# Performance work log

Measured on AMD Instinct MI355X. Metric: run time of the kernel, lower is better.

Reference implementation:

```python
import jax, jax.numpy as jnp
import numpy as np

N_EMBED = 16384
EMBED_DIM = 256
BETA = 1.0  # default forward arg


def setup_inputs() -> dict:
    key = jax.random.key(0)
    k1, k2 = jax.random.split(key)
    z = jax.random.normal(k1, (8, EMBED_DIM, 32, 32), dtype=jnp.float32)
    # nn.Embedding init: uniform(-1/n_embed, 1/n_embed)
    embed_w = jax.random.uniform(k2, (N_EMBED, EMBED_DIM), dtype=jnp.float32,
                                 minval=-1.0 / N_EMBED, maxval=1.0 / N_EMBED)
    return {"z": z, "embed_w": embed_w}


def reference(z, embed_w):
    B, C, H, W = z.shape
    zb = jnp.transpose(z, (0, 2, 3, 1))            # (B,H,W,C)
    zf = zb.reshape(B * H * W, C)                  # (BHW, C)
    # squared L2 distances to every code: ||z||^2 + ||e||^2 - 2 z.e
    d = (jnp.sum(zf ** 2, axis=1, keepdims=True)
         + jnp.sum(embed_w ** 2, axis=1)
         - 2.0 * jnp.einsum('bd,nd->bn', zf, embed_w))  # (BHW, n_embed)
    idx = jnp.argmin(d, axis=1)                    # (BHW,)
    z_q = embed_w[idx].reshape(B, H, W, C)         # codebook gather
    loss = (BETA * jnp.mean((jax.lax.stop_gradient(z_q) - zb) ** 2)
            + jnp.mean((z_q - jax.lax.stop_gradient(zb)) ** 2))
    # straight-through estimator
    z_q = zb + jax.lax.stop_gradient(z_q - zb)
    z_q = jnp.transpose(z_q, (0, 3, 1, 2))         # (B,C,H,W)
    return z_q, loss
```

## Files before the change

kernel.cpp:

```cpp
#include <hip/hip_runtime.h>
#include <hip/hip_bf16.h>
#include <stdint.h>


typedef __attribute__((ext_vector_type(8))) short bf16x8;
typedef __attribute__((ext_vector_type(8))) unsigned short ushort8v;
typedef __attribute__((ext_vector_type(4))) float f32x4;

__device__ __forceinline__ unsigned short f2bf(float f) {
  unsigned u = __float_as_uint(f);
  return (unsigned short)((u + 0x7FFFu + ((u >> 16) & 1u)) >> 16);
}

typedef const __attribute__((address_space(1))) unsigned char* gas1;
typedef __attribute__((address_space(3))) unsigned char* las3;
__device__ __forceinline__ void cp16(const void* g, void* l) {
  __builtin_amdgcn_global_load_lds((gas1)g, (las3)l, 16, 0, 0);
}

__global__ void k_prep(const float* __restrict__ z, const float* __restrict__ ew,
                       unsigned short* __restrict__ zp, unsigned short* __restrict__ ep,
                       float* __restrict__ h2, float* __restrict__ out) {
  __shared__ float tile[32][132];
  int bid = blockIdx.x;
  int t = threadIdx.x;
  if (bid < 512) {
    int b = bid >> 6, ct = (bid >> 3) & 7, hwt = bid & 7;
    const float* src = z + b * 262144 + ct * 32768 + hwt * 128;
#pragma unroll
    for (int it = 0; it < 4; ++it) {
      int cell = it * 1024 + t * 4;
      int cl = cell >> 7, hl = cell & 127;
      float4 v = *(const float4*)(src + cl * 1024 + hl);
      *(float4*)(&tile[cl][hl]) = v;
    }
    __syncthreads();
    int mt = b * 8 + hwt;
    unsigned short* dst = zp + mt * 32768 + ct * 4096;
#pragma unroll
    for (int it = 0; it < 2; ++it) {
      int cell = it * 256 + t;
      int kg = cell >> 7, r = cell & 127;
      ushort8v v;
#pragma unroll
      for (int j = 0; j < 8; ++j) v[j] = f2bf(tile[kg * 8 + j][r]);
      *(ushort8v*)(dst + cell * 8) = v;
    }
  } else {
    if (bid == 512 && t == 0) out[2097152] = 0.0f;
    int n = (bid - 512) * 32 + (t >> 3);
    int nb = n >> 7, col = n & 127;
    float s = 0.0f;
#pragma unroll
    for (int it = 0; it < 4; ++it) {
      int cellk = (t & 7) + it * 8;
      const float4 x = *(const float4*)(ew + n * 256 + cellk * 8);
      const float4 y = *(const float4*)(ew + n * 256 + cellk * 8 + 4);
      s += x.x * x.x + x.y * x.y + x.z * x.z + x.w * x.w
         + y.x * y.x + y.y * y.y + y.z * y.z + y.w * y.w;
      int ks = cellk >> 2, kg = cellk & 3;
      ushort8v v;
      v[0] = f2bf(x.x); v[1] = f2bf(x.y); v[2] = f2bf(x.z); v[3] = f2bf(x.w);
      v[4] = f2bf(y.x); v[5] = f2bf(y.y); v[6] = f2bf(y.z); v[7] = f2bf(y.w);
      *(ushort8v*)(ep + nb * 32768 + ks * 4096 + kg * 1024 + col * 8) = v;
    }
#pragma unroll
    for (int off = 1; off <= 4; off <<= 1) s += __shfl_xor(s, off);
    if ((t & 7) == 0) h2[n] = 0.5f * s;
  }
}

__global__ __launch_bounds__(256, 3) void k_main(
    const unsigned short* __restrict__ zp, const unsigned short* __restrict__ ep,
    const float* __restrict__ h2, int2* __restrict__ partial) {
  __shared__ unsigned char bLds[2][16384];
  int seg = blockIdx.x;
  int mt = blockIdx.y;
  int t = threadIdx.x, wv = t >> 6, lane = t & 63;
  int l15 = lane & 15, kg = lane >> 4;

  bf16x8 av[16];
  const unsigned short* abase = zp + mt * 32768;
#pragma unroll
  for (int m = 0; m < 2; ++m)
#pragma unroll
    for (int ks = 0; ks < 8; ++ks)
      av[m * 8 + ks] = *(const bf16x8*)(abase + ks * 4096 + kg * 1024 +
                                        (wv * 32 + m * 16 + l15) * 8);

  const unsigned char* bsrc = (const unsigned char*)ep + seg * 524288;
  const float* hseg = h2 + seg * 1024;

#pragma unroll
  for (int i = 0; i < 4; ++i)
    cp16(bsrc + i * 4096 + wv * 1024 + lane * 16, &bLds[0][i * 4096 + wv * 1024]);

  f32x4 acc[2][8];
  float best[2][4];
#pragma unroll
  for (int m = 0; m < 2; ++m)
#pragma unroll
    for (int r = 0; r < 4; ++r) best[m][r] = -3.4e38f;

  __syncthreads();

#pragma unroll 4
  for (int s = 0; s < 32; ++s) {
    int cur = s & 1;
    if (s < 31) {
#pragma unroll
      for (int i = 0; i < 4; ++i)
        cp16(bsrc + (s + 1) * 16384 + i * 4096 + wv * 1024 + lane * 16,
             &bLds[cur ^ 1][i * 4096 + wv * 1024]);
    }
    int nb = s >> 2, ph = s & 3;
    if (ph == 0) {
#pragma unroll
      for (int nf = 0; nf < 8; ++nf) {
        float h = hseg[nb * 128 + nf * 16 + l15];
        acc[0][nf] = (f32x4){-h, -h, -h, -h};
        acc[1][nf] = acc[0][nf];
      }
    }
    __builtin_amdgcn_s_setprio(1);
#pragma unroll
    for (int k2 = 0; k2 < 2; ++k2) {
      bf16x8 bv[8];
#pragma unroll
      for (int nf = 0; nf < 8; ++nf)
        bv[nf] = *(const bf16x8*)(&bLds[cur][k2 * 8192 + kg * 2048 + (nf * 16 + l15) * 16]);
#pragma unroll
      for (int m = 0; m < 2; ++m)
#pragma unroll
        for (int nf = 0; nf < 8; ++nf)
          acc[m][nf] = __builtin_amdgcn_mfma_f32_16x16x32_bf16(
              av[m * 8 + ph * 2 + k2], bv[nf], acc[m][nf], 0, 0, 0);
    }
    __builtin_amdgcn_s_setprio(0);
    if (ph == 3) {
      int colbase = nb * 128 + l15;
#pragma unroll
      for (int m = 0; m < 2; ++m)
#pragma unroll
        for (int nf = 0; nf < 8; ++nf) {
          unsigned lcol = (unsigned)(colbase + nf * 16);
#pragma unroll
          for (int r = 0; r < 4; ++r) {
            unsigned p = (__float_as_uint(acc[m][nf][r]) & 0xFFFFF800u) | lcol;
            best[m][r] = fmaxf(best[m][r], __uint_as_float(p));
          }
        }
    }
    __syncthreads();
  }

#pragma unroll
  for (int m = 0; m < 2; ++m)
#pragma unroll
    for (int r = 0; r < 4; ++r) {
      float bvv = best[m][r];
#pragma unroll
      for (int off = 1; off <= 8; off <<= 1) bvv = fmaxf(bvv, __shfl_xor(bvv, off));
      if (l15 == 0) {
        unsigned bits = __float_as_uint(bvv);
        int gidx = seg * 1024 + (int)(bits & 0x7FFu);
        int row = mt * 128 + wv * 32 + m * 16 + kg * 4 + r;
        partial[seg * 8192 + row] = make_int2((int)bits, gidx);
      }
    }
}

__global__ void k_fin(const int2* __restrict__ partial, const float* __restrict__ ew,
                      const float* __restrict__ z, float* __restrict__ out) {
  __shared__ float tile[32][132];
  __shared__ int codeIdx[128];
  int bid = blockIdx.x;
  int b = bid >> 6, hwt = (bid >> 3) & 7, ct = bid & 7;
  int t = threadIdx.x;
  int rowbase = b * 1024 + hwt * 128;
  if (t < 128) {
    int row = rowbase + t;
    float bb = -3.4e38f;
    int bi = 0;
#pragma unroll
    for (int s = 0; s < 16; ++s) {
      int2 p = partial[s * 8192 + row];
      float v = __int_as_float(p.x);
      if (v > bb) { bb = v; bi = p.y; }
    }
    codeIdx[t] = bi;
  }
  __syncthreads();
  int c0 = ct * 32;
  {
    int p = t >> 1, half = t & 1;
    const float* er = ew + codeIdx[p] * 256 + c0 + half * 16;
#pragma unroll
    for (int j = 0; j < 4; ++j) {
      float4 v = *(const float4*)(er + j * 4);
      int c = half * 16 + j * 4;
      tile[c][p] = v.x; tile[c + 1][p] = v.y; tile[c + 2][p] = v.z; tile[c + 3][p] = v.w;
    }
  }
  __syncthreads();
  float ls = 0.0f;
  int obase = b * 262144 + c0 * 1024 + hwt * 128;
#pragma unroll
  for (int it = 0; it < 4; ++it) {
    int c = it * 8 + (t >> 5);
    int p = (t & 31) * 4;
    float4 q = *(const float4*)(&tile[c][p]);
    float4 zv = *(const float4*)(z + obase + c * 1024 + p);
    float dx = q.x - zv.x, dy = q.y - zv.y, dz = q.z - zv.z, dw = q.w - zv.w;
    ls += dx * dx + dy * dy + dz * dz + dw * dw;
    *(float4*)(out + obase + c * 1024 + p) = q;
  }
#pragma unroll
  for (int off = 32; off; off >>= 1) ls += __shfl_xor(ls, off);
  if ((t & 63) == 0) atomicAdd(out + 2097152, ls * (2.0f / 2097152.0f));
}

extern "C" void kernel_launch(void* const* d_in, const int* in_sizes, int n_in,
                              void* d_out, int out_size, void* d_ws, size_t ws_size,
                              hipStream_t stream) {
  const float* z = (const float*)d_in[0];
  const float* ew = (const float*)d_in[1];
  float* out = (float*)d_out;
  unsigned char* ws = (unsigned char*)d_ws;
  unsigned short* zp = (unsigned short*)ws;
  unsigned short* ep = (unsigned short*)(ws + (4u << 20));
  float* h2 = (float*)(ws + (12u << 20));
  int2* partial = (int2*)(ws + (12u << 20) + 65536);

  k_prep<<<1024, 256, 0, stream>>>(z, ew, zp, ep, h2, out);
  k_main<<<dim3(16, 64), 256, 0, stream>>>(zp, ep, h2, partial);
  k_fin<<<512, 256, 0, stream>>>(partial, ew, z, out);
}
```

Baseline: 176.4 us.

## Deepen codebook staging to four-buffer LDS ring with manual waitcnt and barriers

The main kernel's double-buffered LDS staging becomes a 4-slot ring that prefetches three stages ahead, fully unrolled, with explicit vmcnt waits and raw s_barrier in place of __syncthreads. The codebook norm vector is staged into LDS and pre-negated so the accumulator init needs no negation. The finalize kernel is reorganized so each block handles 32 pixels across all 256 channels, reading whole codebook rows contiguously. The aim is to hide global-load latency and cut per-step sync overhead, at the cost of 68KB of LDS per block, lowering occupancy to 2 blocks per CU.

```diff
diff --git a/kernel.cpp b/kernel.cpp
--- a/kernel.cpp
+++ b/kernel.cpp
@@ -14,7 +14,7 @@
 
 typedef const __attribute__((address_space(1))) unsigned char* gas1;
 typedef __attribute__((address_space(3))) unsigned char* las3;
-__device__ __forceinline__ void cp16(const void* g, void* l) {
+__device__ __forceinline__ void cp16g(const void* g, void* l) {
   __builtin_amdgcn_global_load_lds((gas1)g, (las3)l, 16, 0, 0);
 }
 
@@ -66,14 +66,16 @@
     }
 #pragma unroll
     for (int off = 1; off <= 4; off <<= 1) s += __shfl_xor(s, off);
-    if ((t & 7) == 0) h2[n] = 0.5f * s;
-  }
-}
-
-__global__ __launch_bounds__(256, 3) void k_main(
+    if ((t & 7) == 0) h2[n] = -0.5f * s;
+  }
+}
+
+__global__ __launch_bounds__(256, 2) void k_main(
     const unsigned short* __restrict__ zp, const unsigned short* __restrict__ ep,
     const float* __restrict__ h2, int2* __restrict__ partial) {
-  __shared__ unsigned char bLds[2][16384];
+  __shared__ unsigned char lds[4 * 16384 + 4096];
+  unsigned char* ldsring = lds;
+  const float* hLds = (const float*)(lds + 65536);
   int seg = blockIdx.x;
   int mt = blockIdx.y;
   int t = threadIdx.x, wv = t >> 6, lane = t & 63;
@@ -89,11 +91,18 @@
                                         (wv * 32 + m * 16 + l15) * 8);
 
   const unsigned char* bsrc = (const unsigned char*)ep + seg * 524288;
-  const float* hseg = h2 + seg * 1024;
-
-#pragma unroll
-  for (int i = 0; i < 4; ++i)
-    cp16(bsrc + i * 4096 + wv * 1024 + lane * 16, &bLds[0][i * 4096 + wv * 1024]);
+  const unsigned char* bstage = bsrc + wv * 1024 + lane * 16;
+  int ldsw = wv * 1024;
+
+  cp16g((const unsigned char*)(h2 + seg * 1024) + wv * 1024 + lane * 16,
+        lds + 65536 + ldsw);
+#pragma unroll
+  for (int s0 = 0; s0 < 3; ++s0) {
+    const unsigned char* sg = bstage + s0 * 16384;
+    unsigned char* sd = ldsring + s0 * 16384 + ldsw;
+#pragma unroll
+    for (int i = 0; i < 4; ++i) cp16g(sg + i * 4096, sd + i * 4096);
+  }
 
   f32x4 acc[2][8];
   float best[2][4];
@@ -102,57 +111,63 @@
 #pragma unroll
     for (int r = 0; r < 4; ++r) best[m][r] = -3.4e38f;
 
-  __syncthreads();
-
-#pragma unroll 4
-  for (int s = 0; s < 32; ++s) {
-    int cur = s & 1;
-    if (s < 31) {
-#pragma unroll
-      for (int i = 0; i < 4; ++i)
-        cp16(bsrc + (s + 1) * 16384 + i * 4096 + wv * 1024 + lane * 16,
-             &bLds[cur ^ 1][i * 4096 + wv * 1024]);
-    }
-    int nb = s >> 2, ph = s & 3;
-    if (ph == 0) {
-#pragma unroll
-      for (int nf = 0; nf < 8; ++nf) {
-        float h = hseg[nb * 128 + nf * 16 + l15];
-        acc[0][nf] = (f32x4){-h, -h, -h, -h};
-        acc[1][nf] = acc[0][nf];
-      }
-    }
-    __builtin_amdgcn_s_setprio(1);
-#pragma unroll
-    for (int k2 = 0; k2 < 2; ++k2) {
-      bf16x8 bv[8];
-#pragma unroll
-      for (int nf = 0; nf < 8; ++nf)
-        bv[nf] = *(const bf16x8*)(&bLds[cur][k2 * 8192 + kg * 2048 + (nf * 16 + l15) * 16]);
-#pragma unroll
-      for (int m = 0; m < 2; ++m)
-#pragma unroll
-        for (int nf = 0; nf < 8; ++nf)
-          acc[m][nf] = __builtin_amdgcn_mfma_f32_16x16x32_bf16(
-              av[m * 8 + ph * 2 + k2], bv[nf], acc[m][nf], 0, 0, 0);
-    }
-    __builtin_amdgcn_s_setprio(0);
-    if (ph == 3) {
-      int colbase = nb * 128 + l15;
-#pragma unroll
-      for (int m = 0; m < 2; ++m)
-#pragma unroll
-        for (int nf = 0; nf < 8; ++nf) {
-          unsigned lcol = (unsigned)(colbase + nf * 16);
-#pragma unroll
-          for (int r = 0; r < 4; ++r) {
-            unsigned p = (__float_as_uint(acc[m][nf][r]) & 0xFFFFF800u) | lcol;
-            best[m][r] = fmaxf(best[m][r], __uint_as_float(p));
-          }
-        }
-    }
-    __syncthreads();
-  }
+#define STEP(S, VM)                                                              \
+  {                                                                              \
+    if ((S) < 29) {                                                              \
+      const unsigned char* sg = bstage + ((S) + 3) * 16384;                      \
+      unsigned char* sd = ldsring + (((S) + 3) & 3) * 16384 + ldsw;              \
+      cp16g(sg, sd);                                                             \
+      cp16g(sg + 4096, sd + 4096);                                               \
+      cp16g(sg + 8192, sd + 8192);                                               \
+      cp16g(sg + 12288, sd + 12288);                                             \
+    }                                                                            \
+    asm volatile("s_waitcnt vmcnt(" VM ")" ::: "memory");                        \
+    asm volatile("s_barrier" ::: "memory");                                      \
+    {                                                                            \
+      const int nb = (S) >> 2, ph = (S) & 3;                                     \
+      if (ph == 0) {                                                             \
+        _Pragma("unroll") for (int nf = 0; nf < 8; ++nf) {                       \
+          float h = hLds[nb * 128 + nf * 16 + l15];                              \
+          acc[0][nf] = (f32x4){h, h, h, h};                                      \
+          acc[1][nf] = acc[0][nf];                                               \
+        }                                                                        \
+      }                                                                          \
+      const unsigned char* bp = ldsring + ((S) & 3) * 16384 + kg * 2048 + l15 * 16; \
+      __builtin_amdgcn_s_setprio(1);                                             \
+      _Pragma("unroll") for (int k2 = 0; k2 < 2; ++k2) {                         \
+        bf16x8 bv[8];                                                            \
+        _Pragma("unroll") for (int nf = 0; nf < 8; ++nf)                         \
+          bv[nf] = *(const bf16x8*)(bp + k2 * 8192 + nf * 256);                  \
+        _Pragma("unroll") for (int m = 0; m < 2; ++m)                            \
+          _Pragma("unroll") for (int nf = 0; nf < 8; ++nf)                       \
+            acc[m][nf] = __builtin_amdgcn_mfma_f32_16x16x32_bf16(                \
+                av[m * 8 + ph * 2 + k2], bv[nf], acc[m][nf], 0, 0, 0);           \
+      }                                                                          \
+      __builtin_amdgcn_s_setprio(0);                                             \
+      asm volatile("s_barrier" ::: "memory");                                    \
+      if (ph == 3) {                                                             \
+        unsigned colbase = (unsigned)(nb * 128 + l15);                           \
+        _Pragma("unroll") for (int m = 0; m < 2; ++m)                            \
+          _Pragma("unroll") for (int nf = 0; nf < 8; ++nf) {                     \
+            unsigned lcol = colbase + nf * 16u;                                  \
+            _Pragma("unroll") for (int r = 0; r < 4; ++r) {                      \
+              unsigned p = (__float_as_uint(acc[m][nf][r]) & 0xFFFFF800u) | lcol;\
+              best[m][r] = fmaxf(best[m][r], __uint_as_float(p));                \
+            }                                                                    \
+          }                                                                      \
+      }                                                                          \
+    }                                                                            \
+  }
+
+  STEP(0, "12")  STEP(1, "12")  STEP(2, "12")  STEP(3, "12")
+  STEP(4, "12")  STEP(5, "12")  STEP(6, "12")  STEP(7, "12")
+  STEP(8, "12")  STEP(9, "12")  STEP(10, "12") STEP(11, "12")
+  STEP(12, "12") STEP(13, "12") STEP(14, "12") STEP(15, "12")
+  STEP(16, "12") STEP(17, "12") STEP(18, "12") STEP(19, "12")
+  STEP(20, "12") STEP(21, "12") STEP(22, "12") STEP(23, "12")
+  STEP(24, "12") STEP(25, "12") STEP(26, "12") STEP(27, "12")
+  STEP(28, "12") STEP(29, "8")  STEP(30, "4")  STEP(31, "0")
+#undef STEP
 
 #pragma unroll
   for (int m = 0; m < 2; ++m)
@@ -172,14 +187,13 @@
 
 __global__ void k_fin(const int2* __restrict__ partial, const float* __restrict__ ew,
                       const float* __restrict__ z, float* __restrict__ out) {
-  __shared__ float tile[32][132];
-  __shared__ int codeIdx[128];
+  __shared__ float tile[32][260];
+  __shared__ int codeIdx[32];
   int bid = blockIdx.x;
-  int b = bid >> 6, hwt = (bid >> 3) & 7, ct = bid & 7;
-  int t = threadIdx.x;
-  int rowbase = b * 1024 + hwt * 128;
-  if (t < 128) {
-    int row = rowbase + t;
+  int b = bid >> 5, pxt = bid & 31;
+  int t = threadIdx.x, wv = t >> 6, lane = t & 63;
+  if (t < 32) {
+    int row = b * 1024 + pxt * 32 + t;
     float bb = -3.4e38f;
     int bi = 0;
 #pragma unroll
@@ -191,33 +205,31 @@
     codeIdx[t] = bi;
   }
   __syncthreads();
-  int c0 = ct * 32;
-  {
-    int p = t >> 1, half = t & 1;
-    const float* er = ew + codeIdx[p] * 256 + c0 + half * 16;
-#pragma unroll
-    for (int j = 0; j < 4; ++j) {
-      float4 v = *(const float4*)(er + j * 4);
-      int c = half * 16 + j * 4;
-      tile[c][p] = v.x; tile[c + 1][p] = v.y; tile[c + 2][p] = v.z; tile[c + 3][p] = v.w;
-    }
+#pragma unroll
+  for (int i = 0; i < 8; ++i) {
+    int px = wv * 8 + i;
+    int idx = codeIdx[px];
+    float4 v = *(const float4*)(ew + idx * 256 + lane * 4);
+    *(float4*)(&tile[px][lane * 4]) = v;
   }
   __syncthreads();
   float ls = 0.0f;
-  int obase = b * 262144 + c0 * 1024 + hwt * 128;
-#pragma unroll
-  for (int it = 0; it < 4; ++it) {
-    int c = it * 8 + (t >> 5);
-    int p = (t & 31) * 4;
-    float4 q = *(const float4*)(&tile[c][p]);
-    float4 zv = *(const float4*)(z + obase + c * 1024 + p);
+  int zbase = b * 262144 + pxt * 32;
+#pragma unroll
+  for (int j = 0; j < 8; ++j) {
+    int c = wv * 64 + j * 8 + (lane >> 3);
+    int p4 = (lane & 7) * 4;
+    float4 q;
+    q.x = tile[p4][c]; q.y = tile[p4 + 1][c]; q.z = tile[p4 + 2][c]; q.w = tile[p4 + 3][c];
+    const float* zp_ = z + zbase + c * 1024 + p4;
+    float4 zv = *(const float4*)zp_;
     float dx = q.x - zv.x, dy = q.y - zv.y, dz = q.z - zv.z, dw = q.w - zv.w;
     ls += dx * dx + dy * dy + dz * dz + dw * dw;
-    *(float4*)(out + obase + c * 1024 + p) = q;
+    *(float4*)(out + zbase + c * 1024 + p4) = q;
   }
 #pragma unroll
   for (int off = 32; off; off >>= 1) ls += __shfl_xor(ls, off);
-  if ((t & 63) == 0) atomicAdd(out + 2097152, ls * (2.0f / 2097152.0f));
+  if (lane == 0) atomicAdd(out + 2097152, ls * (2.0f / 2097152.0f));
 }
 
 extern "C" void kernel_launch(void* const* d_in, const int* in_sizes, int n_in,
@@ -234,5 +246,5 @@
 
   k_prep<<<1024, 256, 0, stream>>>(z, ew, zp, ep, h2, out);
   k_main<<<dim3(16, 64), 256, 0, stream>>>(zp, ep, h2, partial);
-  k_fin<<<512, 256, 0, stream>>>(partial, ew, z, out);
-}
+  k_fin<<<256, 256, 0, stream>>>(partial, ew, z, out);
+}
```

After: 374.9 us. 113% more time.
